# Performance work log

Measured on AMD Instinct MI355X. Metric: run time of the kernel, lower is better.

## Reference

```python
import jax, jax.numpy as jnp
import numpy as np

LMAX = 2
C1 = 64; C2 = 64; COUT = 64
B = 4096
SUM_RDIM = sum(3**L for L in range(LMAX + 1))   # 13
FEAT1 = C1 * SUM_RDIM                            # 832
FEAT2 = C2 * SUM_RDIM


def _enumerate_paths(Lmax):
    paths = []
    for L1 in range(Lmax + 1):
        for L2 in range(Lmax + 1):
            for k in range(min(L1, L2) + 1):
                Lout = L1 + L2 - 2 * k
                if 0 <= Lout <= Lmax:
                    paths.append((L1, L2, Lout, k, False))
            if L1 >= 1 and L2 >= 1:
                for k in range(min(L1 - 1, L2 - 1) + 1):
                    Lout = L1 + L2 - 2 * k - 1
                    if 0 <= Lout <= Lmax:
                        paths.append((L1, L2, Lout, k, True))
    return paths

PATHS = _enumerate_paths(LMAX)   # 15 paths for Lmax=2


def _path_eq(L1, L2, k, use_eps):
    # Fused equation: W[c,a,b] contracted together with the delta/eps path einsum.
    letters = list('defghijklmnopqrstuvwxyz')  # a,b,c reserved for channels
    i_idx = letters[:L1]
    j_idx = letters[L1:L1 + L2]
    for r in range(k):  # delta: contract last k indices of A with last k of B
        j_idx[L2 - k + r] = i_idx[L1 - k + r]
    i_free = i_idx[:L1 - k]
    j_free = j_idx[:L2 - k]
    eps_sub = None
    if use_eps:  # consume last free index of each side via eps_{p i j}
        p = letters[L1 + L2]
        eps_sub = p + i_free[-1] + j_free[-1]
        i_free, j_free = i_free[:-1], j_free[:-1]
        out = i_free + j_free + [p]
    else:
        out = i_free + j_free
    terms = ['cab', '...a' + ''.join(i_idx), '...b' + ''.join(j_idx)]
    if eps_sub is not None:
        terms.append(eps_sub)
    return ','.join(terms) + '->...c' + ''.join(out)


def _epsilon():
    e = np.zeros((3, 3, 3), dtype=np.float32)
    e[0, 1, 2] = e[1, 2, 0] = e[2, 0, 1] = 1.0
    e[2, 1, 0] = e[1, 0, 2] = e[0, 2, 1] = -1.0
    return jnp.asarray(e)


def _split_by_rank(x, C, Lmax):
    batch = x.shape[:-1]
    out, idx = {}, 0
    for L in range(Lmax + 1):
        d = C * 3**L
        blk = x[..., idx:idx + d]
        idx += d
        out[L] = blk.reshape(*batch, C) if L == 0 else blk.reshape(*batch, C, *((3,) * L))
    return out


def setup_inputs() -> dict:
    key = jax.random.key(0)
    k1, k2, k3 = jax.random.split(key, 3)
    x1 = jax.random.normal(k1, (B, FEAT1), dtype=jnp.float32)
    x2 = jax.random.normal(k2, (B, FEAT2), dtype=jnp.float32)
    weight = jax.random.normal(k3, (len(PATHS) * COUT * C1 * C2,), dtype=jnp.float32) * 0.02
    return {"x1": x1, "x2": x2, "weight": weight}


def reference(x1, x2, weight):
    A = _split_by_rank(x1, C1, LMAX)
    Bt = _split_by_rank(x2, C2, LMAX)
    eps = _epsilon().astype(x1.dtype)
    batch = x1.shape[:-1]
    blocks = {L: jnp.zeros((*batch, COUT) + (3,) * L, dtype=x1.dtype) for L in range(LMAX + 1)}
    wsz = COUT * C1 * C2
    for n, (L1, L2, Lout, k, use_eps) in enumerate(PATHS):
        Wp = weight[n * wsz:(n + 1) * wsz].reshape(COUT, C1, C2)
        eq = _path_eq(L1, L2, k, use_eps)
        ops = (Wp, A[L1], Bt[L2]) + ((eps,) if use_eps else ())
        blocks[Lout] = blocks[Lout] + jnp.einsum(eq, *ops, optimize='optimal')
    parts = [blocks[L].reshape(*batch, COUT * 3**L) for L in range(LMAX + 1)]
    return jnp.concatenate(parts, axis=-1)
```

## Files before the change

### kernel.cpp

```cpp
#include <hip/hip_runtime.h>
#include <cstdint>
#include <cstddef>


#define FEAT 832
#define ZT 64

typedef _Float16 half8 __attribute__((ext_vector_type(8)));
typedef float floatx16 __attribute__((ext_vector_type(16)));

struct Chunk {
  int wbase;
  int o1[3];
  int o2[3];
  float sg[3];
  int d1, d2, nt;
};

__global__ void swz_w_kernel(const float* __restrict__ w, _Float16* __restrict__ o) {
  const int i = blockIdx.x * 256 + threadIdx.x;
  const int lane = i & 63;
  const int pkc  = i >> 6;
  const int cgrp = pkc & 1;
  const int ksg  = (pkc >> 1) & 255;
  const int p    = pkc >> 9;
  const int c  = cgrp * 32 + (lane & 31);
  const int k0 = ksg * 16 + (lane >> 5) * 8;
  const float* src = w + (size_t)p * 262144 + (size_t)c * 4096 + k0;
  const float4 v0 = *(const float4*)(src);
  const float4 v1 = *(const float4*)(src + 4);
  half8 h = { (_Float16)v0.x, (_Float16)v0.y, (_Float16)v0.z, (_Float16)v0.w,
              (_Float16)v1.x, (_Float16)v1.y, (_Float16)v1.z, (_Float16)v1.w };
  *(half8*)(o + (size_t)i * 8) = h;
}

__device__ __forceinline__ half8 splat8(_Float16 h) {
  return half8{h, h, h, h, h, h, h, h};
}

template<int NT>
__device__ __forceinline__ void run_chunk(
    const Chunk C, const int zbase, const int zl, const int hf,
    const int lane, const int tid, const int a0,
    const float* __restrict__ x1, const float* __restrict__ x2,
    const _Float16* __restrict__ Wh,
    _Float16* __restrict__ XS2, _Float16* __restrict__ XS1,
    floatx16& acc0, floatx16& acc1)
{
  __syncthreads();

  #pragma unroll
  for (int t = 0; t < NT; ++t) {
    const size_t base2 = (size_t)zbase * FEAT + C.o2[t];
    for (int e = tid; e < 4096; e += 256) {
      const int zz = e >> 6, b = e & 63;
      XS2[(t * 64 + zz) * 72 + b] =
          (_Float16)x2[base2 + (size_t)zz * FEAT + b * C.d2];
    }
  }
  #pragma unroll
  for (int t = 0; t < NT; ++t) {
    const float sgf = C.sg[t];
    const int o1 = C.o1[t];
    for (int e = tid; e < 4096; e += 256) {
      const int a = e & 63, zz = e >> 6;
      XS1[(t * 64 + a) * 66 + zz] =
          (_Float16)(x1[(size_t)(zbase + zz) * FEAT + o1 + a * C.d1] * sgf);
    }
  }
  __syncthreads();

  half8 x2r[NT][4];
  #pragma unroll
  for (int t = 0; t < NT; ++t) {
    #pragma unroll
    for (int ks = 0; ks < 4; ++ks)
      x2r[t][ks] = *(const half8*)&XS2[(t * 64 + zl) * 72 + ks * 16 + hf * 8];
  }

  const _Float16* __restrict__ Wq = Wh + C.wbase + lane * 8;
  const _Float16* __restrict__ Xq = XS1 + zl;

  half8 afE[2][4], afO[2][4];
  const _Float16* __restrict__ w0 = Wq + (size_t)a0 * 4096;
  #pragma unroll
  for (int ks = 0; ks < 4; ++ks) {
    afE[0][ks] = *(const half8*)(w0 + ks * 1024);
    afE[1][ks] = *(const half8*)(w0 + ks * 1024 + 512);
    afO[0][ks] = *(const half8*)(w0 + 4096 + ks * 1024);
    afO[1][ks] = *(const half8*)(w0 + 4096 + ks * 1024 + 512);
  }
  _Float16 sc[NT], scn[NT];
  #pragma unroll
  for (int t = 0; t < NT; ++t) {
    sc[t]  = Xq[(t * 64 + a0) * 66];
    scn[t] = Xq[(t * 64 + a0 + 1) * 66];
  }

  const int aend = a0 + 32;
  #pragma unroll 1
  for (int a = a0; a < aend; a += 2) {
    {
      half8 sv[NT];
      #pragma unroll
      for (int t = 0; t < NT; ++t) sv[t] = splat8(sc[t]);
      if (a + 2 < aend) {
        #pragma unroll
        for (int t = 0; t < NT; ++t) sc[t] = Xq[(t * 64 + a + 2) * 66];
      }
      half8 tb = sv[0] * x2r[0][0];
      __builtin_amdgcn_s_setprio(1);
      #pragma unroll
      for (int ks = 0; ks < 4; ++ks) {
        tb = sv[0] * x2r[0][ks];
        if (NT > 1) tb += sv[1] * x2r[1][ks];
        if (NT > 2) tb += sv[2] * x2r[2][ks];
        acc0 = __builtin_amdgcn_mfma_f32_32x32x16_f16(afE[0][ks], tb, acc0, 0, 0, 0);
        acc1 = __builtin_amdgcn_mfma_f32_32x32x16_f16(afE[1][ks], tb, acc1, 0, 0, 0);
      }
      __builtin_amdgcn_s_setprio(0);
      if (a + 2 < aend) {
        const _Float16* wn = Wq + (size_t)(a + 2) * 4096;
        #pragma unroll
        for (int ks = 0; ks < 4; ++ks) {
          afE[0][ks] = *(const half8*)(wn + ks * 1024);
          afE[1][ks] = *(const half8*)(wn + ks * 1024 + 512);
        }
      }
    }
    {
      half8 sv[NT];
      #pragma unroll
      for (int t = 0; t < NT; ++t) sv[t] = splat8(scn[t]);
      if (a + 3 < aend) {
        #pragma unroll
        for (int t = 0; t < NT; ++t) scn[t] = Xq[(t * 64 + a + 3) * 66];
      }
      __builtin_amdgcn_s_setprio(1);
      #pragma unroll
      for (int ks = 0; ks < 4; ++ks) {
        half8 tb = sv[0] * x2r[0][ks];
        if (NT > 1) tb += sv[1] * x2r[1][ks];
        if (NT > 2) tb += sv[2] * x2r[2][ks];
        acc0 = __builtin_amdgcn_mfma_f32_32x32x16_f16(afO[0][ks], tb, acc0, 0, 0, 0);
        acc1 = __builtin_amdgcn_mfma_f32_32x32x16_f16(afO[1][ks], tb, acc1, 0, 0, 0);
      }
      __builtin_amdgcn_s_setprio(0);
      if (a + 3 < aend) {
        const _Float16* wn = Wq + (size_t)(a + 3) * 4096;
        #pragma unroll
        for (int ks = 0; ks < 4; ++ks) {
          afO[0][ks] = *(const half8*)(wn + ks * 1024);
          afO[1][ks] = *(const half8*)(wn + ks * 1024 + 512);
        }
      }
    }
  }
}

__global__ __launch_bounds__(256, 2) void tp_kernel(
    const float* __restrict__ x1, const float* __restrict__ x2,
    const _Float16* __restrict__ Wh, float* __restrict__ out)
{
  __shared__ __align__(16) _Float16 XS2[3 * 64 * 72];
  __shared__ __align__(16) _Float16 XS1[3 * 64 * 66];
  __shared__ Chunk chs[7];
  __shared__ int nch_s;

  const int tid  = threadIdx.x;
  const int slot = blockIdx.y;
  const int zbase = blockIdx.x * ZT;
  const int wid  = tid >> 6;
  const int zgrp = wid & 1;
  const int ah   = wid >> 1;
  const int a0   = ah * 32;
  const int lane = tid & 63;
  const int ln31 = lane & 31;
  const int hf   = lane >> 5;
  const int zl   = zgrp * 32 + ln31;

  int offO, dO, mO;
  if (slot == 0)      { offO = 0;   dO = 1; mO = 0; }
  else if (slot < 4)  { offO = 64;  dO = 3; mO = slot - 1; }
  else                { offO = 256; dO = 9; mO = slot - 4; }

  if (tid == 0) {
    int n = 0;
    auto add = [&](int p, int L1, int L2,
                   int i0, int i1, int i2, int j0, int j1, int j2,
                   float s0, float s1, float s2, int nt) {
      const int offs[3] = {0, 64, 256};
      const int ds[3]   = {1, 3, 9};
      Chunk c;
      c.wbase = p * 262144;
      c.o1[0] = offs[L1] + i0; c.o1[1] = offs[L1] + i1; c.o1[2] = offs[L1] + i2;
      c.o2[0] = offs[L2] + j0; c.o2[1] = offs[L2] + j1; c.o2[2] = offs[L2] + j2;
      c.sg[0] = s0; c.sg[1] = s1; c.sg[2] = s2;
      c.d1 = ds[L1]; c.d2 = ds[L2]; c.nt = nt;
      chs[n++] = c;
    };
    if (slot == 0) {
      add(0, 0,0, 0,0,0, 0,0,0, 1,0,0, 1);
      add(5, 1,1, 0,1,2, 0,1,2, 1,1,1, 3);
      add(13,2,2, 0,1,2, 0,1,2, 1,1,1, 3);
      add(13,2,2, 3,4,5, 3,4,5, 1,1,1, 3);
      add(13,2,2, 6,7,8, 6,7,8, 1,1,1, 3);
    } else if (slot < 4) {
      const int m = slot - 1, p1 = (m+1)%3, p2 = (m+2)%3;
      add(1, 0,1, 0,0,0, m,0,0, 1,0,0, 1);
      add(3, 1,0, m,0,0, 0,0,0, 1,0,0, 1);
      add(6, 1,1, p1,p2,0, p2,p1,0, 1,-1,0, 2);
      add(7, 1,2, 0,1,2, 3*m,3*m+1,3*m+2, 1,1,1, 3);
      add(10,2,1, 3*m,3*m+1,3*m+2, 0,1,2, 1,1,1, 3);
      add(14,2,2, 3*p1,3*p1+1,3*p1+2, 3*p2,3*p2+1,3*p2+2, 1,1,1, 3);
      add(14,2,2, 3*p2,3*p2+1,3*p2+2, 3*p1,3*p1+1,3*p1+2, -1,-1,-1, 3);
    } else {
      const int m = slot - 4, u = m/3, v = m%3, q1 = (v+1)%3, q2 = (v+2)%3;
      add(2, 0,2, 0,0,0, m,0,0, 1,0,0, 1);
      add(4, 1,1, u,0,0, v,0,0, 1,0,0, 1);
      add(8, 1,2, q1,q2,0, 3*u+q2,3*u+q1,0, 1,-1,0, 2);
      add(9, 2,0, m,0,0, 0,0,0, 1,0,0, 1);
      add(11,2,1, 3*u+q1,3*u+q2,0, q2,q1,0, 1,-1,0, 2);
      add(12,2,2, 3*u,3*u+1,3*u+2, 3*v,3*v+1,3*v+2, 1,1,1, 3);
    }
    nch_s = n;
  }
  __syncthreads();
  const int nch = nch_s;

  floatx16 acc0, acc1;
  #pragma unroll
  for (int r = 0; r < 16; ++r) { acc0[r] = 0.0f; acc1[r] = 0.0f; }

  for (int ci = 0; ci < nch; ++ci) {
    const Chunk C = chs[ci];
    if (C.nt == 1)      run_chunk<1>(C, zbase, zl, hf, lane, tid, a0, x1, x2, Wh, XS2, XS1, acc0, acc1);
    else if (C.nt == 2) run_chunk<2>(C, zbase, zl, hf, lane, tid, a0, x1, x2, Wh, XS2, XS1, acc0, acc1);
    else                run_chunk<3>(C, zbase, zl, hf, lane, tid, a0, x1, x2, Wh, XS2, XS1, acc0, acc1);
  }

  __syncthreads();
  float* R = (float*)XS2;
  if (ah == 1) {
    #pragma unroll
    for (int r = 0; r < 16; ++r) {
      R[r * 128 + zgrp * 64 + lane]        = acc0[r];
      R[(16 + r) * 128 + zgrp * 64 + lane] = acc1[r];
    }
  }
  __syncthreads();
  if (ah == 0) {
    #pragma unroll
    for (int r = 0; r < 16; ++r) {
      acc0[r] += R[r * 128 + zgrp * 64 + lane];
      acc1[r] += R[(16 + r) * 128 + zgrp * 64 + lane];
    }

    float* __restrict__ op = out + (size_t)(zbase + zl) * FEAT + offO + mO;
    #pragma unroll
    for (int r = 0; r < 16; ++r) {
      const int cr = (r & 3) + 8 * (r >> 2) + 4 * hf;
      op[(size_t)cr * dO]        = acc0[r];
      op[(size_t)(cr + 32) * dO] = acc1[r];
    }
  }
}

extern "C" void kernel_launch(void* const* d_in, const int* in_sizes, int n_in,
                              void* d_out, int out_size, void* d_ws, size_t ws_size,
                              hipStream_t stream) {
  const float* x1 = (const float*)d_in[0];
  const float* x2 = (const float*)d_in[1];
  const float* w  = (const float*)d_in[2];
  float* out = (float*)d_out;
  _Float16* Wh = (_Float16*)d_ws;

  const int nchunks = 15 * 64 * 4096 / 8;
  hipLaunchKernelGGL(swz_w_kernel, dim3(nchunks / 256), dim3(256), 0, stream, w, Wh);

  dim3 grid(64, 13);
  hipLaunchKernelGGL(tp_kernel, grid, dim3(256), 0, stream, x1, x2, Wh, out);
}
```

Baseline: 373.5 us.

## Stage full x2 tile in LDS once, read x1 directly, split work across 8 waves

New measurement: 527.2 us. 1.41x slower.

```diff
diff --git a/kernel.cpp b/kernel.cpp
--- a/kernel.cpp
+++ b/kernel.cpp
@@ -5,8 +5,10 @@
 
 #define FEAT 832
 #define ZT 64
+#define X2S 834
 
 typedef _Float16 half8 __attribute__((ext_vector_type(8)));
+typedef _Float16 half2v __attribute__((ext_vector_type(2)));
 typedef float floatx16 __attribute__((ext_vector_type(16)));
 
 struct Chunk {
@@ -38,132 +40,126 @@
   return half8{h, h, h, h, h, h, h, h};
 }
 
-template<int NT>
+template<int NT, int D2>
 __device__ __forceinline__ void run_chunk(
-    const Chunk C, const int zbase, const int zl, const int hf,
-    const int lane, const int tid, const int a0,
-    const float* __restrict__ x1, const float* __restrict__ x2,
-    const _Float16* __restrict__ Wh,
-    _Float16* __restrict__ XS2, _Float16* __restrict__ XS1,
+    const Chunk C, const int zbase, const int ln31, const int hf,
+    const int lane, const int cg, const int a0,
+    const float* __restrict__ x1, const _Float16* __restrict__ Wh,
+    const _Float16* __restrict__ X2,
     floatx16& acc0, floatx16& acc1)
 {
-  __syncthreads();
-
+  half8 x2r[NT][2][4];
   #pragma unroll
   for (int t = 0; t < NT; ++t) {
-    const size_t base2 = (size_t)zbase * FEAT + C.o2[t];
-    for (int e = tid; e < 4096; e += 256) {
-      const int zz = e >> 6, b = e & 63;
-      XS2[(t * 64 + zz) * 72 + b] =
-          (_Float16)x2[base2 + (size_t)zz * FEAT + b * C.d2];
-    }
-  }
-  #pragma unroll
-  for (int t = 0; t < NT; ++t) {
-    const float sgf = C.sg[t];
-    const int o1 = C.o1[t];
-    for (int e = tid; e < 4096; e += 256) {
-      const int a = e & 63, zz = e >> 6;
-      XS1[(t * 64 + a) * 66 + zz] =
-          (_Float16)(x1[(size_t)(zbase + zz) * FEAT + o1 + a * C.d1] * sgf);
-    }
-  }
-  __syncthreads();
-
-  half8 x2r[NT][4];
-  #pragma unroll
-  for (int t = 0; t < NT; ++t) {
-    #pragma unroll
-    for (int ks = 0; ks < 4; ++ks)
-      x2r[t][ks] = *(const half8*)&XS2[(t * 64 + zl) * 72 + ks * 16 + hf * 8];
-  }
-
-  const _Float16* __restrict__ Wq = Wh + C.wbase + lane * 8;
-  const _Float16* __restrict__ Xq = XS1 + zl;
-
-  half8 afE[2][4], afO[2][4];
+    #pragma unroll
+    for (int zg = 0; zg < 2; ++zg) {
+      const _Float16* row = X2 + (zg * 32 + ln31) * X2S + C.o2[t] + hf * 8 * D2;
+      #pragma unroll
+      for (int ks = 0; ks < 4; ++ks) {
+        half8 v;
+        #pragma unroll
+        for (int j = 0; j < 8; ++j) v[j] = row[(ks * 16 + j) * D2];
+        x2r[t][zg][ks] = v;
+      }
+    }
+  }
+
+  const _Float16* __restrict__ Wq = Wh + C.wbase + cg * 512 + lane * 8;
+  const float* __restrict__ x1r0 = x1 + (size_t)(zbase + ln31) * FEAT;
+  const float* __restrict__ x1r1 = x1 + (size_t)(zbase + 32 + ln31) * FEAT;
+
+  half8 afE[4], afO[4];
   const _Float16* __restrict__ w0 = Wq + (size_t)a0 * 4096;
   #pragma unroll
   for (int ks = 0; ks < 4; ++ks) {
-    afE[0][ks] = *(const half8*)(w0 + ks * 1024);
-    afE[1][ks] = *(const half8*)(w0 + ks * 1024 + 512);
-    afO[0][ks] = *(const half8*)(w0 + 4096 + ks * 1024);
-    afO[1][ks] = *(const half8*)(w0 + 4096 + ks * 1024 + 512);
-  }
-  _Float16 sc[NT], scn[NT];
+    afE[ks] = *(const half8*)(w0 + ks * 1024);
+    afO[ks] = *(const half8*)(w0 + 4096 + ks * 1024);
+  }
+  float sc[NT][2], scn[NT][2];
   #pragma unroll
   for (int t = 0; t < NT; ++t) {
-    sc[t]  = Xq[(t * 64 + a0) * 66];
-    scn[t] = Xq[(t * 64 + a0 + 1) * 66];
-  }
-
-  const int aend = a0 + 32;
+    const int o1 = C.o1[t];
+    sc[t][0]  = x1r0[o1 + a0 * C.d1];
+    sc[t][1]  = x1r1[o1 + a0 * C.d1];
+    scn[t][0] = x1r0[o1 + (a0 + 1) * C.d1];
+    scn[t][1] = x1r1[o1 + (a0 + 1) * C.d1];
+  }
+
+  const int aend = a0 + 16;
   #pragma unroll 1
   for (int a = a0; a < aend; a += 2) {
     {
-      half8 sv[NT];
-      #pragma unroll
-      for (int t = 0; t < NT; ++t) sv[t] = splat8(sc[t]);
+      half8 sv[NT][2];
+      #pragma unroll
+      for (int t = 0; t < NT; ++t) {
+        sv[t][0] = splat8((_Float16)(sc[t][0] * C.sg[t]));
+        sv[t][1] = splat8((_Float16)(sc[t][1] * C.sg[t]));
+      }
       if (a + 2 < aend) {
         #pragma unroll
-        for (int t = 0; t < NT; ++t) sc[t] = Xq[(t * 64 + a + 2) * 66];
-      }
-      half8 tb = sv[0] * x2r[0][0];
+        for (int t = 0; t < NT; ++t) {
+          sc[t][0] = x1r0[C.o1[t] + (a + 2) * C.d1];
+          sc[t][1] = x1r1[C.o1[t] + (a + 2) * C.d1];
+        }
+      }
       __builtin_amdgcn_s_setprio(1);
       #pragma unroll
       for (int ks = 0; ks < 4; ++ks) {
-        tb = sv[0] * x2r[0][ks];
-        if (NT > 1) tb += sv[1] * x2r[1][ks];
-        if (NT > 2) tb += sv[2] * x2r[2][ks];
-        acc0 = __builtin_amdgcn_mfma_f32_32x32x16_f16(afE[0][ks], tb, acc0, 0, 0, 0);
-        acc1 = __builtin_amdgcn_mfma_f32_32x32x16_f16(afE[1][ks], tb, acc1, 0, 0, 0);
+        half8 tb0 = sv[0][0] * x2r[0][0][ks];
+        half8 tb1 = sv[0][1] * x2r[0][1][ks];
+        if (NT > 1) { tb0 += sv[1][0] * x2r[1][0][ks]; tb1 += sv[1][1] * x2r[1][1][ks]; }
+        if (NT > 2) { tb0 += sv[2][0] * x2r[2][0][ks]; tb1 += sv[2][1] * x2r[2][1][ks]; }
+        acc0 = __builtin_amdgcn_mfma_f32_32x32x16_f16(afE[ks], tb0, acc0, 0, 0, 0);
+        acc1 = __builtin_amdgcn_mfma_f32_32x32x16_f16(afE[ks], tb1, acc1, 0, 0, 0);
       }
       __builtin_amdgcn_s_setprio(0);
       if (a + 2 < aend) {
         const _Float16* wn = Wq + (size_t)(a + 2) * 4096;
         #pragma unroll
-        for (int ks = 0; ks < 4; ++ks) {
-          afE[0][ks] = *(const half8*)(wn + ks * 1024);
-          afE[1][ks] = *(const half8*)(wn + ks * 1024 + 512);
+        for (int ks = 0; ks < 4; ++ks)
+          afE[ks] = *(const half8*)(wn + ks * 1024);
+      }
+    }
+    {
+      half8 sv[NT][2];
+      #pragma unroll
+      for (int t = 0; t < NT; ++t) {
+        sv[t][0] = splat8((_Float16)(scn[t][0] * C.sg[t]));
+        sv[t][1] = splat8((_Float16)(scn[t][1] * C.sg[t]));
+      }
+      if (a + 3 < aend) {
+        #pragma unroll
+        for (int t = 0; t < NT; ++t) {
+          scn[t][0] = x1r0[C.o1[t] + (a + 3) * C.d1];
+          scn[t][1] = x1r1[C.o1[t] + (a + 3) * C.d1];
         }
       }
-    }
-    {
-      half8 sv[NT];
-      #pragma unroll
-      for (int t = 0; t < NT; ++t) sv[t] = splat8(scn[t]);
-      if (a + 3 < aend) {
-        #pragma unroll
-        for (int t = 0; t < NT; ++t) scn[t] = Xq[(t * 64 + a + 3) * 66];
-      }
       __builtin_amdgcn_s_setprio(1);
       #pragma unroll
       for (int ks = 0; ks < 4; ++ks) {
-        half8 tb = sv[0] * x2r[0][ks];
-        if (NT > 1) tb += sv[1] * x2r[1][ks];
-        if (NT > 2) tb += sv[2] * x2r[2][ks];
-        acc0 = __builtin_amdgcn_mfma_f32_32x32x16_f16(afO[0][ks], tb, acc0, 0, 0, 0);
-        acc1 = __builtin_amdgcn_mfma_f32_32x32x16_f16(afO[1][ks], tb, acc1, 0, 0, 0);
+        half8 tb0 = sv[0][0] * x2r[0][0][ks];
+        half8 tb1 = sv[0][1] * x2r[0][1][ks];
+        if (NT > 1) { tb0 += sv[1][0] * x2r[1][0][ks]; tb1 += sv[1][1] * x2r[1][1][ks]; }
+        if (NT > 2) { tb0 += sv[2][0] * x2r[2][0][ks]; tb1 += sv[2][1] * x2r[2][1][ks]; }
+        acc0 = __builtin_amdgcn_mfma_f32_32x32x16_f16(afO[ks], tb0, acc0, 0, 0, 0);
+        acc1 = __builtin_amdgcn_mfma_f32_32x32x16_f16(afO[ks], tb1, acc1, 0, 0, 0);
       }
       __builtin_amdgcn_s_setprio(0);
       if (a + 3 < aend) {
         const _Float16* wn = Wq + (size_t)(a + 3) * 4096;
         #pragma unroll
-        for (int ks = 0; ks < 4; ++ks) {
-          afO[0][ks] = *(const half8*)(wn + ks * 1024);
-          afO[1][ks] = *(const half8*)(wn + ks * 1024 + 512);
-        }
-      }
-    }
-  }
-}
-
-__global__ __launch_bounds__(256, 2) void tp_kernel(
+        for (int ks = 0; ks < 4; ++ks)
+          afO[ks] = *(const half8*)(wn + ks * 1024);
+      }
+    }
+  }
+}
+
+__global__ __launch_bounds__(512, 2) void tp_kernel(
     const float* __restrict__ x1, const float* __restrict__ x2,
     const _Float16* __restrict__ Wh, float* __restrict__ out)
 {
-  __shared__ __align__(16) _Float16 XS2[3 * 64 * 72];
-  __shared__ __align__(16) _Float16 XS1[3 * 64 * 66];
+  __shared__ __align__(16) _Float16 X2[64 * X2S];
   __shared__ Chunk chs[7];
   __shared__ int nch_s;
 
@@ -171,13 +167,12 @@
   const int slot = blockIdx.y;
   const int zbase = blockIdx.x * ZT;
   const int wid  = tid >> 6;
-  const int zgrp = wid & 1;
-  const int ah   = wid >> 1;
-  const int a0   = ah * 32;
+  const int cg   = wid & 1;
+  const int aq   = wid >> 1;
+  const int a0   = aq * 16;
   const int lane = tid & 63;
   const int ln31 = lane & 31;
   const int hf   = lane >> 5;
-  const int zl   = zgrp * 32 + ln31;
 
   int offO, dO, mO;
   if (slot == 0)      { offO = 0;   dO = 1; mO = 0; }
@@ -225,6 +220,20 @@
     }
     nch_s = n;
   }
+
+  for (int row = wid; row < 64; row += 8) {
+    const float* __restrict__ src = x2 + (size_t)(zbase + row) * FEAT;
+    _Float16* __restrict__ dst = X2 + row * X2S;
+    #pragma unroll
+    for (int k = 0; k < 7; ++k) {
+      const int f = k * 128 + lane * 2;
+      if (f < FEAT) {
+        const float2 v = *(const float2*)(src + f);
+        half2v h = { (_Float16)v.x, (_Float16)v.y };
+        *(half2v*)(dst + f) = h;
+      }
+    }
+  }
   __syncthreads();
   const int nch = nch_s;
 
@@ -234,34 +243,46 @@
 
   for (int ci = 0; ci < nch; ++ci) {
     const Chunk C = chs[ci];
-    if (C.nt == 1)      run_chunk<1>(C, zbase, zl, hf, lane, tid, a0, x1, x2, Wh, XS2, XS1, acc0, acc1);
-    else if (C.nt == 2) run_chunk<2>(C, zbase, zl, hf, lane, tid, a0, x1, x2, Wh, XS2, XS1, acc0, acc1);
-    else                run_chunk<3>(C, zbase, zl, hf, lane, tid, a0, x1, x2, Wh, XS2, XS1, acc0, acc1);
+    const int key = C.nt * 16 + C.d2;
+    switch (key) {
+      case 17: run_chunk<1,1>(C, zbase, ln31, hf, lane, cg, a0, x1, Wh, X2, acc0, acc1); break;
+      case 19: run_chunk<1,3>(C, zbase, ln31, hf, lane, cg, a0, x1, Wh, X2, acc0, acc1); break;
+      case 25: run_chunk<1,9>(C, zbase, ln31, hf, lane, cg, a0, x1, Wh, X2, acc0, acc1); break;
+      case 35: run_chunk<2,3>(C, zbase, ln31, hf, lane, cg, a0, x1, Wh, X2, acc0, acc1); break;
+      case 41: run_chunk<2,9>(C, zbase, ln31, hf, lane, cg, a0, x1, Wh, X2, acc0, acc1); break;
+      case 51: run_chunk<3,3>(C, zbase, ln31, hf, lane, cg, a0, x1, Wh, X2, acc0, acc1); break;
+      default: run_chunk<3,9>(C, zbase, ln31, hf, lane, cg, a0, x1, Wh, X2, acc0, acc1); break;
+    }
   }
 
   __syncthreads();
-  float* R = (float*)XS2;
-  if (ah == 1) {
+  float* Dv = (float*)X2;
+  if (aq > 0) {
+    const int b = (cg * 3 + (aq - 1)) * 2048;
     #pragma unroll
     for (int r = 0; r < 16; ++r) {
-      R[r * 128 + zgrp * 64 + lane]        = acc0[r];
-      R[(16 + r) * 128 + zgrp * 64 + lane] = acc1[r];
+      Dv[b + r * 64 + lane]        = acc0[r];
+      Dv[b + 1024 + r * 64 + lane] = acc1[r];
     }
   }
   __syncthreads();
-  if (ah == 0) {
+  if (aq == 0) {
+    #pragma unroll
+    for (int j = 0; j < 3; ++j) {
+      const int b = (cg * 3 + j) * 2048;
+      #pragma unroll
+      for (int r = 0; r < 16; ++r) {
+        acc0[r] += Dv[b + r * 64 + lane];
+        acc1[r] += Dv[b + 1024 + r * 64 + lane];
+      }
+    }
+    float* __restrict__ op0 = out + (size_t)(zbase + ln31) * FEAT + offO + mO;
+    float* __restrict__ op1 = out + (size_t)(zbase + 32 + ln31) * FEAT + offO + mO;
     #pragma unroll
     for (int r = 0; r < 16; ++r) {
-      acc0[r] += R[r * 128 + zgrp * 64 + lane];
-      acc1[r] += R[(16 + r) * 128 + zgrp * 64 + lane];
-    }
-
-    float* __restrict__ op = out + (size_t)(zbase + zl) * FEAT + offO + mO;
-    #pragma unroll
-    for (int r = 0; r < 16; ++r) {
-      const int cr = (r & 3) + 8 * (r >> 2) + 4 * hf;
-      op[(size_t)cr * dO]        = acc0[r];
-      op[(size_t)(cr + 32) * dO] = acc1[r];
+      const int cr = cg * 32 + (r & 3) + 8 * (r >> 2) + 4 * hf;
+      op0[(size_t)cr * dO] = acc0[r];
+      op1[(size_t)cr * dO] = acc1[r];
     }
   }
 }
@@ -279,5 +300,5 @@
   hipLaunchKernelGGL(swz_w_kernel, dim3(nchunks / 256), dim3(256), 0, stream, w, Wh);
 
   dim3 grid(64, 13);
-  hipLaunchKernelGGL(tp_kernel, grid, dim3(256), 0, stream, x1, x2, Wh, out);
-}
+  hipLaunchKernelGGL(tp_kernel, grid, dim3(512), 0, stream, x1, x2, Wh, out);
+}
```

## Prefetch next chunk inputs into registers and double the waves per block

Applied to the files above, without the earlier changes.

Measured after the change: 479.8 us. 1.28x slower.

```diff
diff --git a/kernel.cpp b/kernel.cpp
--- a/kernel.cpp
+++ b/kernel.cpp
@@ -38,38 +38,57 @@
   return half8{h, h, h, h, h, h, h, h};
 }
 
+struct StageRegs {
+  float r2[3][8];
+  float r1[3][8];
+};
+
+__device__ __forceinline__ void issue_loads(
+    const Chunk& C, const int zbase, const int tid,
+    const float* __restrict__ x1, const float* __restrict__ x2, StageRegs& S)
+{
+  #pragma unroll
+  for (int t = 0; t < 3; ++t) {
+    if (t < C.nt) {
+      const int o2 = C.o2[t], o1 = C.o1[t];
+      #pragma unroll
+      for (int k = 0; k < 8; ++k) {
+        const int e = tid + k * 512;
+        const int zz = e >> 6, b = e & 63;
+        const size_t row = (size_t)(zbase + zz) * FEAT;
+        S.r2[t][k] = x2[row + o2 + b * C.d2];
+        S.r1[t][k] = x1[row + o1 + b * C.d1];
+      }
+    }
+  }
+}
+
+__device__ __forceinline__ void write_stage(
+    const Chunk& C, const int tid, const StageRegs& S,
+    _Float16* __restrict__ XS2, _Float16* __restrict__ XS1)
+{
+  #pragma unroll
+  for (int t = 0; t < 3; ++t) {
+    if (t < C.nt) {
+      const float sg = C.sg[t];
+      #pragma unroll
+      for (int k = 0; k < 8; ++k) {
+        const int e = tid + k * 512;
+        const int zz = e >> 6, b = e & 63;
+        XS2[(t * 64 + zz) * 72 + b] = (_Float16)S.r2[t][k];
+        XS1[(t * 64 + b) * 66 + zz] = (_Float16)(S.r1[t][k] * sg);
+      }
+    }
+  }
+}
+
 template<int NT>
-__device__ __forceinline__ void run_chunk(
-    const Chunk C, const int zbase, const int zl, const int hf,
-    const int lane, const int tid, const int a0,
-    const float* __restrict__ x1, const float* __restrict__ x2,
+__device__ __forceinline__ void run_compute(
+    const Chunk C, const int zl, const int hf, const int lane, const int a0,
     const _Float16* __restrict__ Wh,
-    _Float16* __restrict__ XS2, _Float16* __restrict__ XS1,
+    const _Float16* __restrict__ XS2, const _Float16* __restrict__ XS1,
     floatx16& acc0, floatx16& acc1)
 {
-  __syncthreads();
-
-  #pragma unroll
-  for (int t = 0; t < NT; ++t) {
-    const size_t base2 = (size_t)zbase * FEAT + C.o2[t];
-    for (int e = tid; e < 4096; e += 256) {
-      const int zz = e >> 6, b = e & 63;
-      XS2[(t * 64 + zz) * 72 + b] =
-          (_Float16)x2[base2 + (size_t)zz * FEAT + b * C.d2];
-    }
-  }
-  #pragma unroll
-  for (int t = 0; t < NT; ++t) {
-    const float sgf = C.sg[t];
-    const int o1 = C.o1[t];
-    for (int e = tid; e < 4096; e += 256) {
-      const int a = e & 63, zz = e >> 6;
-      XS1[(t * 64 + a) * 66 + zz] =
-          (_Float16)(x1[(size_t)(zbase + zz) * FEAT + o1 + a * C.d1] * sgf);
-    }
-  }
-  __syncthreads();
-
   half8 x2r[NT][4];
   #pragma unroll
   for (int t = 0; t < NT; ++t) {
@@ -97,7 +116,7 @@
     scn[t] = Xq[(t * 64 + a0 + 1) * 66];
   }
 
-  const int aend = a0 + 32;
+  const int aend = a0 + 16;
   #pragma unroll 1
   for (int a = a0; a < aend; a += 2) {
     {
@@ -108,11 +127,10 @@
         #pragma unroll
         for (int t = 0; t < NT; ++t) sc[t] = Xq[(t * 64 + a + 2) * 66];
       }
-      half8 tb = sv[0] * x2r[0][0];
       __builtin_amdgcn_s_setprio(1);
       #pragma unroll
       for (int ks = 0; ks < 4; ++ks) {
-        tb = sv[0] * x2r[0][ks];
+        half8 tb = sv[0] * x2r[0][ks];
         if (NT > 1) tb += sv[1] * x2r[1][ks];
         if (NT > 2) tb += sv[2] * x2r[2][ks];
         acc0 = __builtin_amdgcn_mfma_f32_32x32x16_f16(afE[0][ks], tb, acc0, 0, 0, 0);
@@ -158,12 +176,13 @@
   }
 }
 
-__global__ __launch_bounds__(256, 2) void tp_kernel(
+__global__ __launch_bounds__(512, 2) void tp_kernel(
     const float* __restrict__ x1, const float* __restrict__ x2,
     const _Float16* __restrict__ Wh, float* __restrict__ out)
 {
-  __shared__ __align__(16) _Float16 XS2[3 * 64 * 72];
-  __shared__ __align__(16) _Float16 XS1[3 * 64 * 66];
+  __shared__ __align__(16) char SH[52992];
+  _Float16* __restrict__ XS2 = (_Float16*)SH;
+  _Float16* __restrict__ XS1 = (_Float16*)(SH + 27648);
   __shared__ Chunk chs[7];
   __shared__ int nch_s;
 
@@ -172,8 +191,8 @@
   const int zbase = blockIdx.x * ZT;
   const int wid  = tid >> 6;
   const int zgrp = wid & 1;
-  const int ah   = wid >> 1;
-  const int a0   = ah * 32;
+  const int aq   = wid >> 1;
+  const int a0   = aq * 16;
   const int lane = tid & 63;
   const int ln31 = lane & 31;
   const int hf   = lane >> 5;
@@ -232,30 +251,48 @@
   #pragma unroll
   for (int r = 0; r < 16; ++r) { acc0[r] = 0.0f; acc1[r] = 0.0f; }
 
-  for (int ci = 0; ci < nch; ++ci) {
+  const int rot = blockIdx.x % nch;
+  StageRegs S;
+  issue_loads(chs[rot], zbase, tid, x1, x2, S);
+
+  for (int k = 0; k < nch; ++k) {
+    const int ci = (k + rot) < nch ? (k + rot) : (k + rot - nch);
     const Chunk C = chs[ci];
-    if (C.nt == 1)      run_chunk<1>(C, zbase, zl, hf, lane, tid, a0, x1, x2, Wh, XS2, XS1, acc0, acc1);
-    else if (C.nt == 2) run_chunk<2>(C, zbase, zl, hf, lane, tid, a0, x1, x2, Wh, XS2, XS1, acc0, acc1);
-    else                run_chunk<3>(C, zbase, zl, hf, lane, tid, a0, x1, x2, Wh, XS2, XS1, acc0, acc1);
+    __syncthreads();
+    write_stage(C, tid, S, XS2, XS1);
+    __syncthreads();
+    if (k + 1 < nch) {
+      const int cn = (ci + 1) < nch ? (ci + 1) : 0;
+      issue_loads(chs[cn], zbase, tid, x1, x2, S);
+    }
+    if (C.nt == 1)      run_compute<1>(C, zl, hf, lane, a0, Wh, XS2, XS1, acc0, acc1);
+    else if (C.nt == 2) run_compute<2>(C, zl, hf, lane, a0, Wh, XS2, XS1, acc0, acc1);
+    else                run_compute<3>(C, zl, hf, lane, a0, Wh, XS2, XS1, acc0, acc1);
   }
 
   __syncthreads();
-  float* R = (float*)XS2;
-  if (ah == 1) {
+  float* __restrict__ Dv = (float*)SH;
+  if (aq > 0) {
+    const int b0 = (((aq - 1) * 2 + zgrp) * 2 + 0) * 1024;
+    const int b1 = (((aq - 1) * 2 + zgrp) * 2 + 1) * 1024;
     #pragma unroll
     for (int r = 0; r < 16; ++r) {
-      R[r * 128 + zgrp * 64 + lane]        = acc0[r];
-      R[(16 + r) * 128 + zgrp * 64 + lane] = acc1[r];
+      Dv[b0 + r * 64 + lane] = acc0[r];
+      Dv[b1 + r * 64 + lane] = acc1[r];
     }
   }
   __syncthreads();
-  if (ah == 0) {
+  if (aq == 0) {
     #pragma unroll
-    for (int r = 0; r < 16; ++r) {
-      acc0[r] += R[r * 128 + zgrp * 64 + lane];
-      acc1[r] += R[(16 + r) * 128 + zgrp * 64 + lane];
-    }
-
+    for (int j = 1; j < 4; ++j) {
+      const int b0 = (((j - 1) * 2 + zgrp) * 2 + 0) * 1024;
+      const int b1 = (((j - 1) * 2 + zgrp) * 2 + 1) * 1024;
+      #pragma unroll
+      for (int r = 0; r < 16; ++r) {
+        acc0[r] += Dv[b0 + r * 64 + lane];
+        acc1[r] += Dv[b1 + r * 64 + lane];
+      }
+    }
     float* __restrict__ op = out + (size_t)(zbase + zl) * FEAT + offO + mO;
     #pragma unroll
     for (int r = 0; r < 16; ++r) {
@@ -279,5 +316,5 @@
   hipLaunchKernelGGL(swz_w_kernel, dim3(nchunks / 256), dim3(256), 0, stream, w, Wh);
 
   dim3 grid(64, 13);
-  hipLaunchKernelGGL(tp_kernel, grid, dim3(256), 0, stream, x1, x2, Wh, out);
-}
+  hipLaunchKernelGGL(tp_kernel, grid, dim3(512), 0, stream, x1, x2, Wh, out);
+}
```

## Stage full x2 tile once in LDS, split K over 8 waves, swizzle block order

Applied to the files above, without the earlier changes.

After: 450.6 us. 1.21x slower.

```diff
diff --git a/kernel.cpp b/kernel.cpp
--- a/kernel.cpp
+++ b/kernel.cpp
@@ -4,9 +4,10 @@
 
 
 #define FEAT 832
-#define ZT 64
+#define X2S 834
 
 typedef _Float16 half8 __attribute__((ext_vector_type(8)));
+typedef _Float16 half2v __attribute__((ext_vector_type(2)));
 typedef float floatx16 __attribute__((ext_vector_type(16)));
 
 struct Chunk {
@@ -38,44 +39,24 @@
   return half8{h, h, h, h, h, h, h, h};
 }
 
-template<int NT>
+template<int NT, int D2>
 __device__ __forceinline__ void run_chunk(
-    const Chunk C, const int zbase, const int zl, const int hf,
-    const int lane, const int tid, const int a0,
-    const float* __restrict__ x1, const float* __restrict__ x2,
+    const Chunk C, const int zl, const int hf, const int lane, const int a0,
     const _Float16* __restrict__ Wh,
-    _Float16* __restrict__ XS2, _Float16* __restrict__ XS1,
+    const _Float16* __restrict__ X2, const _Float16* __restrict__ XS1,
     floatx16& acc0, floatx16& acc1)
 {
-  __syncthreads();
-
-  #pragma unroll
-  for (int t = 0; t < NT; ++t) {
-    const size_t base2 = (size_t)zbase * FEAT + C.o2[t];
-    for (int e = tid; e < 4096; e += 256) {
-      const int zz = e >> 6, b = e & 63;
-      XS2[(t * 64 + zz) * 72 + b] =
-          (_Float16)x2[base2 + (size_t)zz * FEAT + b * C.d2];
-    }
-  }
-  #pragma unroll
-  for (int t = 0; t < NT; ++t) {
-    const float sgf = C.sg[t];
-    const int o1 = C.o1[t];
-    for (int e = tid; e < 4096; e += 256) {
-      const int a = e & 63, zz = e >> 6;
-      XS1[(t * 64 + a) * 66 + zz] =
-          (_Float16)(x1[(size_t)(zbase + zz) * FEAT + o1 + a * C.d1] * sgf);
-    }
-  }
-  __syncthreads();
-
   half8 x2r[NT][4];
   #pragma unroll
   for (int t = 0; t < NT; ++t) {
-    #pragma unroll
-    for (int ks = 0; ks < 4; ++ks)
-      x2r[t][ks] = *(const half8*)&XS2[(t * 64 + zl) * 72 + ks * 16 + hf * 8];
+    const _Float16* __restrict__ row = X2 + zl * X2S + C.o2[t] + hf * 8 * D2;
+    #pragma unroll
+    for (int ks = 0; ks < 4; ++ks) {
+      half8 v;
+      #pragma unroll
+      for (int j = 0; j < 8; ++j) v[j] = row[(ks * 16 + j) * D2];
+      x2r[t][ks] = v;
+    }
   }
 
   const _Float16* __restrict__ Wq = Wh + C.wbase + lane * 8;
@@ -97,7 +78,7 @@
     scn[t] = Xq[(t * 64 + a0 + 1) * 66];
   }
 
-  const int aend = a0 + 32;
+  const int aend = a0 + 16;
   #pragma unroll 1
   for (int a = a0; a < aend; a += 2) {
     {
@@ -108,11 +89,10 @@
         #pragma unroll
         for (int t = 0; t < NT; ++t) sc[t] = Xq[(t * 64 + a + 2) * 66];
       }
-      half8 tb = sv[0] * x2r[0][0];
       __builtin_amdgcn_s_setprio(1);
       #pragma unroll
       for (int ks = 0; ks < 4; ++ks) {
-        tb = sv[0] * x2r[0][ks];
+        half8 tb = sv[0] * x2r[0][ks];
         if (NT > 1) tb += sv[1] * x2r[1][ks];
         if (NT > 2) tb += sv[2] * x2r[2][ks];
         acc0 = __builtin_amdgcn_mfma_f32_32x32x16_f16(afE[0][ks], tb, acc0, 0, 0, 0);
@@ -158,26 +138,28 @@
   }
 }
 
-__global__ __launch_bounds__(256, 2) void tp_kernel(
+__global__ __launch_bounds__(512, 2) void tp_kernel(
     const float* __restrict__ x1, const float* __restrict__ x2,
     const _Float16* __restrict__ Wh, float* __restrict__ out)
 {
-  __shared__ __align__(16) _Float16 XS2[3 * 64 * 72];
+  __shared__ __align__(16) _Float16 X2[64 * X2S];
   __shared__ __align__(16) _Float16 XS1[3 * 64 * 66];
   __shared__ Chunk chs[7];
   __shared__ int nch_s;
 
   const int tid  = threadIdx.x;
-  const int slot = blockIdx.y;
-  const int zbase = blockIdx.x * ZT;
+  const int bid  = blockIdx.x;
+  const int u    = (bid & 7) * 104 + (bid >> 3);
+  const int slot = u >> 6;
+  const int zbase = (u & 63) * 64;
   const int wid  = tid >> 6;
-  const int zgrp = wid & 1;
-  const int ah   = wid >> 1;
-  const int a0   = ah * 32;
+  const int zg   = wid & 1;
+  const int aq   = wid >> 1;
+  const int a0   = aq * 16;
   const int lane = tid & 63;
   const int ln31 = lane & 31;
   const int hf   = lane >> 5;
-  const int zl   = zgrp * 32 + ln31;
+  const int zl   = zg * 32 + ln31;
 
   int offO, dO, mO;
   if (slot == 0)      { offO = 0;   dO = 1; mO = 0; }
@@ -215,15 +197,29 @@
       add(14,2,2, 3*p1,3*p1+1,3*p1+2, 3*p2,3*p2+1,3*p2+2, 1,1,1, 3);
       add(14,2,2, 3*p2,3*p2+1,3*p2+2, 3*p1,3*p1+1,3*p1+2, -1,-1,-1, 3);
     } else {
-      const int m = slot - 4, u = m/3, v = m%3, q1 = (v+1)%3, q2 = (v+2)%3;
+      const int m = slot - 4, uu = m/3, v = m%3, q1 = (v+1)%3, q2 = (v+2)%3;
       add(2, 0,2, 0,0,0, m,0,0, 1,0,0, 1);
-      add(4, 1,1, u,0,0, v,0,0, 1,0,0, 1);
-      add(8, 1,2, q1,q2,0, 3*u+q2,3*u+q1,0, 1,-1,0, 2);
+      add(4, 1,1, uu,0,0, v,0,0, 1,0,0, 1);
+      add(8, 1,2, q1,q2,0, 3*uu+q2,3*uu+q1,0, 1,-1,0, 2);
       add(9, 2,0, m,0,0, 0,0,0, 1,0,0, 1);
-      add(11,2,1, 3*u+q1,3*u+q2,0, q2,q1,0, 1,-1,0, 2);
-      add(12,2,2, 3*u,3*u+1,3*u+2, 3*v,3*v+1,3*v+2, 1,1,1, 3);
+      add(11,2,1, 3*uu+q1,3*uu+q2,0, q2,q1,0, 1,-1,0, 2);
+      add(12,2,2, 3*uu,3*uu+1,3*uu+2, 3*v,3*v+1,3*v+2, 1,1,1, 3);
     }
     nch_s = n;
+  }
+
+  for (int row = wid; row < 64; row += 8) {
+    const float* __restrict__ src = x2 + (size_t)(zbase + row) * FEAT;
+    _Float16* __restrict__ dst = X2 + row * X2S;
+    #pragma unroll
+    for (int k = 0; k < 7; ++k) {
+      const int f = k * 128 + lane * 2;
+      if (f < FEAT) {
+        const float2 v = *(const float2*)(src + f);
+        half2v h = { (_Float16)v.x, (_Float16)v.y };
+        *(half2v*)(dst + f) = h;
+      }
+    }
   }
   __syncthreads();
   const int nch = nch_s;
@@ -234,28 +230,56 @@
 
   for (int ci = 0; ci < nch; ++ci) {
     const Chunk C = chs[ci];
-    if (C.nt == 1)      run_chunk<1>(C, zbase, zl, hf, lane, tid, a0, x1, x2, Wh, XS2, XS1, acc0, acc1);
-    else if (C.nt == 2) run_chunk<2>(C, zbase, zl, hf, lane, tid, a0, x1, x2, Wh, XS2, XS1, acc0, acc1);
-    else                run_chunk<3>(C, zbase, zl, hf, lane, tid, a0, x1, x2, Wh, XS2, XS1, acc0, acc1);
+    __syncthreads();
+    #pragma unroll
+    for (int t = 0; t < 3; ++t) {
+      if (t < C.nt) {
+        const float sgf = C.sg[t];
+        const int o1 = C.o1[t];
+        for (int e = tid; e < 4096; e += 512) {
+          const int a = e & 63, zz = e >> 6;
+          XS1[(t * 64 + a) * 66 + zz] =
+              (_Float16)(x1[(size_t)(zbase + zz) * FEAT + o1 + a * C.d1] * sgf);
+        }
+      }
+    }
+    __syncthreads();
+
+    const int key = C.nt * 16 + C.d2;
+    switch (key) {
+      case 17: run_chunk<1,1>(C, zl, hf, lane, a0, Wh, X2, XS1, acc0, acc1); break;
+      case 19: run_chunk<1,3>(C, zl, hf, lane, a0, Wh, X2, XS1, acc0, acc1); break;
+      case 25: run_chunk<1,9>(C, zl, hf, lane, a0, Wh, X2, XS1, acc0, acc1); break;
+      case 35: run_chunk<2,3>(C, zl, hf, lane, a0, Wh, X2, XS1, acc0, acc1); break;
+      case 41: run_chunk<2,9>(C, zl, hf, lane, a0, Wh, X2, XS1, acc0, acc1); break;
+      case 51: run_chunk<3,3>(C, zl, hf, lane, a0, Wh, X2, XS1, acc0, acc1); break;
+      default: run_chunk<3,9>(C, zl, hf, lane, a0, Wh, X2, XS1, acc0, acc1); break;
+    }
   }
 
   __syncthreads();
-  float* R = (float*)XS2;
-  if (ah == 1) {
+  float* __restrict__ Dv = (float*)X2;
+  if (aq > 0) {
+    const int b0 = (((aq - 1) * 2 + zg) * 2 + 0) * 1024;
+    const int b1 = (((aq - 1) * 2 + zg) * 2 + 1) * 1024;
     #pragma unroll
     for (int r = 0; r < 16; ++r) {
-      R[r * 128 + zgrp * 64 + lane]        = acc0[r];
-      R[(16 + r) * 128 + zgrp * 64 + lane] = acc1[r];
+      Dv[b0 + r * 64 + lane] = acc0[r];
+      Dv[b1 + r * 64 + lane] = acc1[r];
     }
   }
   __syncthreads();
-  if (ah == 0) {
-    #pragma unroll
-    for (int r = 0; r < 16; ++r) {
-      acc0[r] += R[r * 128 + zgrp * 64 + lane];
-      acc1[r] += R[(16 + r) * 128 + zgrp * 64 + lane];
-    }
-
+  if (aq == 0) {
+    #pragma unroll
+    for (int j = 1; j < 4; ++j) {
+      const int b0 = (((j - 1) * 2 + zg) * 2 + 0) * 1024;
+      const int b1 = (((j - 1) * 2 + zg) * 2 + 1) * 1024;
+      #pragma unroll
+      for (int r = 0; r < 16; ++r) {
+        acc0[r] += Dv[b0 + r * 64 + lane];
+        acc1[r] += Dv[b1 + r * 64 + lane];
+      }
+    }
     float* __restrict__ op = out + (size_t)(zbase + zl) * FEAT + offO + mO;
     #pragma unroll
     for (int r = 0; r < 16; ++r) {
@@ -278,6 +302,5 @@
   const int nchunks = 15 * 64 * 4096 / 8;
   hipLaunchKernelGGL(swz_w_kernel, dim3(nchunks / 256), dim3(256), 0, stream, w, Wh);
 
-  dim3 grid(64, 13);
-  hipLaunchKernelGGL(tp_kernel, grid, dim3(256), 0, stream, x1, x2, Wh, out);
-}
+  hipLaunchKernelGGL(tp_kernel, dim3(832), dim3(512), 0, stream, x1, x2, Wh, out);
+}
```
